# Optimization experiments

Measured on AMD Instinct MI355X. Metric: run time of the kernel, lower is better.

## Reference

```python
import jax, jax.numpy as jnp
import numpy as np

VOCAB, EMB, HID = 128000, 128, 1024
B, S = 4, 4096

def setup_inputs() -> dict:
    key = jax.random.key(0)
    k1, k2, k3 = jax.random.split(key, 3)
    x = jax.random.randint(k1, (B, S), 0, VOCAB, dtype=jnp.int64)
    embed_vocab = jax.random.normal(k2, (VOCAB, EMB), dtype=jnp.float32)
    embed_hidden = jax.random.normal(k3, (EMB, HID), dtype=jnp.float32)
    return {"x": x, "embed_vocab": embed_vocab, "embed_hidden": embed_hidden}

def reference(x, embed_vocab, embed_hidden):
    # Faithful to the torch module: build the full factorized table [V,H]
    # then gather rows by token id (F.embedding with defaults: no padding_idx,
    # no max_norm).
    table = embed_vocab @ embed_hidden          # [V, H]
    return jnp.take(table, x, axis=0)           # [B, S, H]
```

## Files before the change

kernel.cpp:

```cpp
#include <hip/hip_runtime.h>


using f32x4 = __attribute__((ext_vector_type(4))) float;
using i32x4 = __attribute__((ext_vector_type(4))) int;
typedef unsigned int u32;

constexpr int EMB = 128;
constexpr int HID = 1024;

__device__ inline void cvt8(const float f[8], i32x4& hi, i32x4& lo) {
    u32 h[8], l[8];
#pragma unroll
    for (int e = 0; e < 8; ++e) {
        u32 fb = __float_as_uint(f[e]);
        u32 hb = fb & 0xFFFF0000u;
        float r = f[e] - __uint_as_float(hb);
        u32 lb = __float_as_uint(r) & 0xFFFF0000u;
        h[e] = hb; l[e] = lb;
    }
#pragma unroll
    for (int p = 0; p < 4; ++p) {
        hi[p] = (int)((h[2*p] >> 16) | h[2*p+1]);
        lo[p] = (int)((l[2*p] >> 16) | l[2*p+1]);
    }
}

__device__ inline f32x4 mfma_bf16(i32x4 a, i32x4 b, f32x4 c) {
    f32x4 d;
    asm volatile("v_mfma_f32_16x16x32_bf16 %0, %1, %2, %3"
                 : "=&v"(d) : "v"(a), "v"(b), "v"(c));
    return d;
}

__device__ inline void gload16(const u32* src, u32* ldsdst) {
    __builtin_amdgcn_global_load_lds(
        (const __attribute__((address_space(1))) u32*)src,
        (__attribute__((address_space(3))) u32*)ldsdst, 16, 0, 0);
}

__global__ void prep_eh(const float* __restrict__ eh, u32* __restrict__ wsBh,
                        u32* __restrict__ wsBl) {
    const int t  = blockIdx.x * 256 + threadIdx.x;
    const int n  = t >> 4, k8 = t & 15;
    float f[8];
#pragma unroll
    for (int j = 0; j < 8; ++j) f[j] = eh[(k8*8 + j)*HID + n];
    i32x4 hi, lo; cvt8(f, hi, lo);
    const int s = k8 >> 2, gs = (k8 & 3) ^ ((n >> 1) & 3);
    const int off = (s*HID + n)*16 + gs*4;
    *(i32x4*)(wsBh + off) = hi;
    *(i32x4*)(wsBl + off) = lo;
}

__global__ void prep_ev(const int* __restrict__ x, const float* __restrict__ ev,
                        u32* __restrict__ wsAh, u32* __restrict__ wsAl, int M) {
    const int t = blockIdx.x * 256 + threadIdx.x;
    const int m = t >> 4, k8 = t & 15;
    const long id = x[m];
    const float* src = ev + id * EMB + k8*8;
    float f[8];
    *(float4*)(f)     = *(const float4*)(src);
    *(float4*)(f + 4) = *(const float4*)(src + 4);
    i32x4 hi, lo; cvt8(f, hi, lo);
    const int s = k8 >> 2, gs = (k8 & 3) ^ ((m >> 1) & 3);
    const long off = ((long)s*M + m)*16 + gs*4;
    *(i32x4*)(wsAh + off) = hi;
    *(i32x4*)(wsAl + off) = lo;
}

__global__ __launch_bounds__(256, 2)
void femb_main(const u32* __restrict__ wsAh, const u32* __restrict__ wsAl,
               const u32* __restrict__ wsBh, const u32* __restrict__ wsBl,
               float* __restrict__ out, int mtiles, int M)
{
    __shared__ __align__(16) u32 lds[2][4][2048];

    const int tid  = threadIdx.x;
    const int lane = tid & 63, wid = tid >> 6;
    const int bid  = blockIdx.x;
    const int mt   = bid % mtiles;
    const int nt   = bid / mtiles;
    const long m0  = (long)mt * 128, n0 = (long)nt * 128;
    const int wm   = wid >> 1, wn = wid & 1;
    const int rl   = lane & 15, g = lane >> 4;

    const int row_ = wid*32 + (lane >> 2);
    const int gr_  = lane & 3;

    f32x4 acc[4][4];
#pragma unroll
    for (int i = 0; i < 4; ++i)
#pragma unroll
        for (int j = 0; j < 4; ++j) acc[i][j] = (f32x4){0.f, 0.f, 0.f, 0.f};

    auto stage = [&](int s, int buf) {
#pragma unroll
        for (int j = 0; j < 2; ++j) {
            const int  r  = row_ + j*16;
            const int  lo = wid*512 + j*256;
            const long ao = ((long)s*M   + m0 + r)*16 + gr_*4;
            const long bo = ((long)s*HID + n0 + r)*16 + gr_*4;
            gload16(wsAh + ao, &lds[buf][0][lo]);
            gload16(wsAl + ao, &lds[buf][1][lo]);
            gload16(wsBh + bo, &lds[buf][2][lo]);
            gload16(wsBl + bo, &lds[buf][3][lo]);
        }
    };

    auto compute = [&](int buf) {
        i32x4 bh[4], bl[4];
#pragma unroll
        for (int nf = 0; nf < 4; ++nf) {
            const int nr  = wn*64 + nf*16 + rl;
            const int off = nr*16 + ((g ^ ((nr >> 1) & 3)) << 2);
            bh[nf] = *(const i32x4*)&lds[buf][2][off];
            bl[nf] = *(const i32x4*)&lds[buf][3][off];
        }
#pragma unroll
        for (int mf = 0; mf < 4; ++mf) {
            const int mr  = wm*64 + mf*16 + rl;
            const int off = mr*16 + ((g ^ ((mr >> 1) & 3)) << 2);
            const i32x4 ah = *(const i32x4*)&lds[buf][0][off];
            const i32x4 al = *(const i32x4*)&lds[buf][1][off];
#pragma unroll
            for (int nf = 0; nf < 4; ++nf) {
                acc[mf][nf] = mfma_bf16(ah, bh[nf], acc[mf][nf]);
                acc[mf][nf] = mfma_bf16(ah, bl[nf], acc[mf][nf]);
                acc[mf][nf] = mfma_bf16(al, bh[nf], acc[mf][nf]);
            }
        }
    };

    stage(0, 0);
    for (int s = 0; s < 4; ++s) {
        __builtin_amdgcn_s_waitcnt(0);
        __syncthreads();
        if (s < 3) stage(s + 1, (s + 1) & 1);
        compute(s & 1);
    }

#pragma unroll
    for (int mf = 0; mf < 4; ++mf)
#pragma unroll
        for (int j = 0; j < 4; ++j) {
            const long row = m0 + wm*64 + mf*16 + g*4 + j;
            float* dst = out + row * HID + n0 + wn*64 + rl;
#pragma unroll
            for (int nf = 0; nf < 4; ++nf) dst[nf * 16] = acc[mf][nf][j];
        }
}

extern "C" void kernel_launch(void* const* d_in, const int* in_sizes, int n_in,
                              void* d_out, int out_size, void* d_ws, size_t ws_size,
                              hipStream_t stream) {
    const int*   x   = (const int*)d_in[0];
    const float* ev  = (const float*)d_in[1];
    const float* eh  = (const float*)d_in[2];
    float*       out = (float*)d_out;

    const int M      = in_sizes[0];
    const int mtiles = M / 128;

    u32* wsBh = (u32*)d_ws;
    u32* wsBl = wsBh + (size_t)HID*64;
    u32* wsAh = wsBl + (size_t)HID*64;
    u32* wsAl = wsAh + (size_t)M*64;
    if (ws_size < (size_t)(2*HID*64 + 2*(size_t)M*64) * 4) return;

    prep_eh<<<HID*16/256, 256, 0, stream>>>(eh, wsBh, wsBl);
    prep_ev<<<M*16/256, 256, 0, stream>>>(x, ev, wsAh, wsAl, M);
    femb_main<<<mtiles * (HID/128), 256, 0, stream>>>(wsAh, wsAl, wsBh, wsBl,
                                                      out, mtiles, M);
}
```

Measured before the change: 123.6 us.

## Merge prep kernels and enlarge GEMM tiles to 256x256 with 1024-thread blocks

The two preprocessing kernels become one launch that splits blocks between the embedding-gather path and the hidden-weight conversion path, removing one kernel launch. The main kernel moves from 128x128 tiles with 4 waves to 256x256 tiles with 16 waves per block, doubling LDS use and reusing each staged operand across more MFMAs. Block indices are remapped so groups of 8 M-tiles share N-tiles, for better L2 locality. The trade-off is fewer, larger blocks (256 total), which may underfill the CUs and limit occupancy, since only one block fits per CU.

```diff
diff --git a/kernel.cpp b/kernel.cpp
--- a/kernel.cpp
+++ b/kernel.cpp
@@ -38,54 +38,54 @@
         (__attribute__((address_space(3))) u32*)ldsdst, 16, 0, 0);
 }
 
-__global__ void prep_eh(const float* __restrict__ eh, u32* __restrict__ wsBh,
-                        u32* __restrict__ wsBl) {
-    const int t  = blockIdx.x * 256 + threadIdx.x;
-    const int n  = t >> 4, k8 = t & 15;
-    float f[8];
+__global__ void prep_all(const int* __restrict__ x, const float* __restrict__ ev,
+                         const float* __restrict__ eh,
+                         u32* __restrict__ wsAh, u32* __restrict__ wsAl,
+                         u32* __restrict__ wsBh, u32* __restrict__ wsBl, int M) {
+    const int bid = blockIdx.x;
+    const int evblocks = M >> 4;
+    if (bid < evblocks) {
+        const int t = bid * 256 + threadIdx.x;
+        const int m = t >> 4, k8 = t & 15;
+        const long id = x[m];
+        const float* src = ev + id * EMB + k8 * 8;
+        float f[8];
+        *(float4*)(f)     = *(const float4*)(src);
+        *(float4*)(f + 4) = *(const float4*)(src + 4);
+        i32x4 hi, lo; cvt8(f, hi, lo);
+        const int s = k8 >> 2, gs = (k8 & 3) ^ ((m >> 1) & 3);
+        const long off = ((long)s * M + m) * 16 + gs * 4;
+        *(i32x4*)(wsAh + off) = hi;
+        *(i32x4*)(wsAl + off) = lo;
+    } else {
+        const int t = (bid - evblocks) * 256 + threadIdx.x;
+        const int n = t >> 4, k8 = t & 15;
+        float f[8];
 #pragma unroll
-    for (int j = 0; j < 8; ++j) f[j] = eh[(k8*8 + j)*HID + n];
-    i32x4 hi, lo; cvt8(f, hi, lo);
-    const int s = k8 >> 2, gs = (k8 & 3) ^ ((n >> 1) & 3);
-    const int off = (s*HID + n)*16 + gs*4;
-    *(i32x4*)(wsBh + off) = hi;
-    *(i32x4*)(wsBl + off) = lo;
+        for (int j = 0; j < 8; ++j) f[j] = eh[(k8 * 8 + j) * HID + n];
+        i32x4 hi, lo; cvt8(f, hi, lo);
+        const int s = k8 >> 2, gs = (k8 & 3) ^ ((n >> 1) & 3);
+        const int off = (s * HID + n) * 16 + gs * 4;
+        *(i32x4*)(wsBh + off) = hi;
+        *(i32x4*)(wsBl + off) = lo;
+    }
 }
 
-__global__ void prep_ev(const int* __restrict__ x, const float* __restrict__ ev,
-                        u32* __restrict__ wsAh, u32* __restrict__ wsAl, int M) {
-    const int t = blockIdx.x * 256 + threadIdx.x;
-    const int m = t >> 4, k8 = t & 15;
-    const long id = x[m];
-    const float* src = ev + id * EMB + k8*8;
-    float f[8];
-    *(float4*)(f)     = *(const float4*)(src);
-    *(float4*)(f + 4) = *(const float4*)(src + 4);
-    i32x4 hi, lo; cvt8(f, hi, lo);
-    const int s = k8 >> 2, gs = (k8 & 3) ^ ((m >> 1) & 3);
-    const long off = ((long)s*M + m)*16 + gs*4;
-    *(i32x4*)(wsAh + off) = hi;
-    *(i32x4*)(wsAl + off) = lo;
-}
-
-__global__ __launch_bounds__(256, 2)
+__global__ __launch_bounds__(1024, 1)
 void femb_main(const u32* __restrict__ wsAh, const u32* __restrict__ wsAl,
                const u32* __restrict__ wsBh, const u32* __restrict__ wsBl,
-               float* __restrict__ out, int mtiles, int M)
+               float* __restrict__ out, int M)
 {
-    __shared__ __align__(16) u32 lds[2][4][2048];
+    __shared__ __align__(16) u32 lds[2][4][4096];
 
     const int tid  = threadIdx.x;
     const int lane = tid & 63, wid = tid >> 6;
-    const int bid  = blockIdx.x;
-    const int mt   = bid % mtiles;
-    const int nt   = bid / mtiles;
-    const long m0  = (long)mt * 128, n0 = (long)nt * 128;
-    const int wm   = wid >> 1, wn = wid & 1;
-    const int rl   = lane & 15, g = lane >> 4;
-
-    const int row_ = wid*32 + (lane >> 2);
-    const int gr_  = lane & 3;
+    const int bid = blockIdx.x;
+    const int mh  = bid >> 5, r5 = bid & 31;
+    const int nt  = r5 >> 3,  mt = mh * 8 + (r5 & 7);
+    const long m0 = (long)mt * 256, n0 = (long)nt * 256;
+    const int wm  = wid >> 2, wn = wid & 3;
+    const int rl  = lane & 15, g = lane >> 4;
 
     f32x4 acc[4][4];
 #pragma unroll
@@ -94,32 +94,27 @@
         for (int j = 0; j < 4; ++j) acc[i][j] = (f32x4){0.f, 0.f, 0.f, 0.f};
 
     auto stage = [&](int s, int buf) {
-#pragma unroll
-        for (int j = 0; j < 2; ++j) {
-            const int  r  = row_ + j*16;
-            const int  lo = wid*512 + j*256;
-            const long ao = ((long)s*M   + m0 + r)*16 + gr_*4;
-            const long bo = ((long)s*HID + n0 + r)*16 + gr_*4;
-            gload16(wsAh + ao, &lds[buf][0][lo]);
-            gload16(wsAl + ao, &lds[buf][1][lo]);
-            gload16(wsBh + bo, &lds[buf][2][lo]);
-            gload16(wsBl + bo, &lds[buf][3][lo]);
-        }
+        const long ao = ((long)s * M   + m0) * 16 + tid * 4;
+        const long bo = ((long)s * HID + n0) * 16 + tid * 4;
+        gload16(wsAh + ao, &lds[buf][0][tid * 4]);
+        gload16(wsAl + ao, &lds[buf][1][tid * 4]);
+        gload16(wsBh + bo, &lds[buf][2][tid * 4]);
+        gload16(wsBl + bo, &lds[buf][3][tid * 4]);
     };
 
     auto compute = [&](int buf) {
         i32x4 bh[4], bl[4];
 #pragma unroll
         for (int nf = 0; nf < 4; ++nf) {
-            const int nr  = wn*64 + nf*16 + rl;
-            const int off = nr*16 + ((g ^ ((nr >> 1) & 3)) << 2);
+            const int nr  = wn * 64 + nf * 16 + rl;
+            const int off = nr * 16 + ((g ^ ((nr >> 1) & 3)) << 2);
             bh[nf] = *(const i32x4*)&lds[buf][2][off];
             bl[nf] = *(const i32x4*)&lds[buf][3][off];
         }
 #pragma unroll
         for (int mf = 0; mf < 4; ++mf) {
-            const int mr  = wm*64 + mf*16 + rl;
-            const int off = mr*16 + ((g ^ ((mr >> 1) & 3)) << 2);
+            const int mr  = wm * 64 + mf * 16 + rl;
+            const int off = mr * 16 + ((g ^ ((mr >> 1) & 3)) << 2);
             const i32x4 ah = *(const i32x4*)&lds[buf][0][off];
             const i32x4 al = *(const i32x4*)&lds[buf][1][off];
 #pragma unroll
@@ -143,8 +138,8 @@
     for (int mf = 0; mf < 4; ++mf)
 #pragma unroll
         for (int j = 0; j < 4; ++j) {
-            const long row = m0 + wm*64 + mf*16 + g*4 + j;
-            float* dst = out + row * HID + n0 + wn*64 + rl;
+            const long row = m0 + wm * 64 + mf * 16 + g * 4 + j;
+            float* dst = out + row * HID + n0 + wn * 64 + rl;
 #pragma unroll
             for (int nf = 0; nf < 4; ++nf) dst[nf * 16] = acc[mf][nf][j];
         }
@@ -158,17 +153,16 @@
     const float* eh  = (const float*)d_in[2];
     float*       out = (float*)d_out;
 
-    const int M      = in_sizes[0];
-    const int mtiles = M / 128;
+    const int M = in_sizes[0];
 
     u32* wsBh = (u32*)d_ws;
-    u32* wsBl = wsBh + (size_t)HID*64;
-    u32* wsAh = wsBl + (size_t)HID*64;
-    u32* wsAl = wsAh + (size_t)M*64;
-    if (ws_size < (size_t)(2*HID*64 + 2*(size_t)M*64) * 4) return;
+    u32* wsBl = wsBh + (size_t)HID * 64;
+    u32* wsAh = wsBl + (size_t)HID * 64;
+    u32* wsAl = wsAh + (size_t)M * 64;
+    if (ws_size < (size_t)(2 * HID * 64 + 2 * (size_t)M * 64) * 4) return;
 
-    prep_eh<<<HID*16/256, 256, 0, stream>>>(eh, wsBh, wsBl);
-    prep_ev<<<M*16/256, 256, 0, stream>>>(x, ev, wsAh, wsAl, M);
-    femb_main<<<mtiles * (HID/128), 256, 0, stream>>>(wsAh, wsAl, wsBh, wsBl,
-                                                      out, mtiles, M);
+    prep_all<<<(M >> 4) + (HID * 16 / 256), 256, 0, stream>>>(
+        x, ev, eh, wsAh, wsAl, wsBh, wsBl, M);
+    femb_main<<<(M / 256) * (HID / 256), 1024, 0, stream>>>(
+        wsAh, wsAl, wsBh, wsBl, out, M);
 }
```

Result: slower. 126.7 us (+2.5%).

## Fuse gather and bf16 split conversion into main GEMM kernel, drop prep passes

Applied to the files above, without the earlier changes.

Removes the two prep kernels that wrote split-bf16 hi/lo copies of the gathered embedding rows and the hidden matrix to workspace. The main kernel now gathers fp32 rows by token id, loads columns of embed_hidden, converts them to hi/lo in registers, and writes them to LDS. Global loads for the next stage are issued before the MFMA compute and stored to LDS after it, so the pipeline moves from async global-to-LDS copies to register staging. This saves two launches and the workspace round trip. The cost is redundant conversion across the 8 N-tiles, strided uncoalesced column reads of embed_hidden, and higher register pressure.

```diff
diff --git a/kernel.cpp b/kernel.cpp
--- a/kernel.cpp
+++ b/kernel.cpp
@@ -32,46 +32,9 @@
     return d;
 }
 
-__device__ inline void gload16(const u32* src, u32* ldsdst) {
-    __builtin_amdgcn_global_load_lds(
-        (const __attribute__((address_space(1))) u32*)src,
-        (__attribute__((address_space(3))) u32*)ldsdst, 16, 0, 0);
-}
-
-__global__ void prep_eh(const float* __restrict__ eh, u32* __restrict__ wsBh,
-                        u32* __restrict__ wsBl) {
-    const int t  = blockIdx.x * 256 + threadIdx.x;
-    const int n  = t >> 4, k8 = t & 15;
-    float f[8];
-#pragma unroll
-    for (int j = 0; j < 8; ++j) f[j] = eh[(k8*8 + j)*HID + n];
-    i32x4 hi, lo; cvt8(f, hi, lo);
-    const int s = k8 >> 2, gs = (k8 & 3) ^ ((n >> 1) & 3);
-    const int off = (s*HID + n)*16 + gs*4;
-    *(i32x4*)(wsBh + off) = hi;
-    *(i32x4*)(wsBl + off) = lo;
-}
-
-__global__ void prep_ev(const int* __restrict__ x, const float* __restrict__ ev,
-                        u32* __restrict__ wsAh, u32* __restrict__ wsAl, int M) {
-    const int t = blockIdx.x * 256 + threadIdx.x;
-    const int m = t >> 4, k8 = t & 15;
-    const long id = x[m];
-    const float* src = ev + id * EMB + k8*8;
-    float f[8];
-    *(float4*)(f)     = *(const float4*)(src);
-    *(float4*)(f + 4) = *(const float4*)(src + 4);
-    i32x4 hi, lo; cvt8(f, hi, lo);
-    const int s = k8 >> 2, gs = (k8 & 3) ^ ((m >> 1) & 3);
-    const long off = ((long)s*M + m)*16 + gs*4;
-    *(i32x4*)(wsAh + off) = hi;
-    *(i32x4*)(wsAl + off) = lo;
-}
-
 __global__ __launch_bounds__(256, 2)
-void femb_main(const u32* __restrict__ wsAh, const u32* __restrict__ wsAl,
-               const u32* __restrict__ wsBh, const u32* __restrict__ wsBl,
-               float* __restrict__ out, int mtiles, int M)
+void femb(const int* __restrict__ x, const float* __restrict__ ev,
+          const float* __restrict__ eh, float* __restrict__ out, int mtiles)
 {
     __shared__ __align__(16) u32 lds[2][4][2048];
 
@@ -84,8 +47,49 @@
     const int wm   = wid >> 1, wn = wid & 1;
     const int rl   = lane & 15, g = lane >> 4;
 
-    const int row_ = wid*32 + (lane >> 2);
-    const int gr_  = lane & 3;
+    const int r0 = tid >> 2, aoct = tid & 3;
+    const float* abase0 = ev + (long)x[m0 + r0]      * EMB + aoct * 8;
+    const float* abase1 = ev + (long)x[m0 + 64 + r0] * EMB + aoct * 8;
+    const int bn = tid & 127, boct0 = tid >> 7;
+    const float* bcol = eh + n0 + bn;
+
+    float af[2][8], bf[2][8];
+
+    auto loads = [&](int s) {
+        const int k0 = s * 32;
+#pragma unroll
+        for (int h = 0; h < 2; ++h) {
+            const float* src = (h ? abase1 : abase0) + k0;
+            *(float4*)(&af[h][0]) = *(const float4*)(src);
+            *(float4*)(&af[h][4]) = *(const float4*)(src + 4);
+        }
+#pragma unroll
+        for (int h = 0; h < 2; ++h) {
+            const int ko = k0 + (boct0 + 2 * h) * 8;
+#pragma unroll
+            for (int j = 0; j < 8; ++j)
+                bf[h][j] = bcol[(long)(ko + j) * HID];
+        }
+    };
+
+    auto cvtwrite = [&](int buf) {
+#pragma unroll
+        for (int h = 0; h < 2; ++h) {
+            i32x4 hi, lo; cvt8(af[h], hi, lo);
+            const int r  = r0 + h * 64;
+            const int gs = aoct ^ ((r >> 1) & 3);
+            *(i32x4*)&lds[buf][0][r * 16 + gs * 4] = hi;
+            *(i32x4*)&lds[buf][1][r * 16 + gs * 4] = lo;
+        }
+#pragma unroll
+        for (int h = 0; h < 2; ++h) {
+            i32x4 hi, lo; cvt8(bf[h], hi, lo);
+            const int o  = boct0 + 2 * h;
+            const int gs = o ^ ((bn >> 1) & 3);
+            *(i32x4*)&lds[buf][2][bn * 16 + gs * 4] = hi;
+            *(i32x4*)&lds[buf][3][bn * 16 + gs * 4] = lo;
+        }
+    };
 
     f32x4 acc[4][4];
 #pragma unroll
@@ -93,33 +97,19 @@
 #pragma unroll
         for (int j = 0; j < 4; ++j) acc[i][j] = (f32x4){0.f, 0.f, 0.f, 0.f};
 
-    auto stage = [&](int s, int buf) {
-#pragma unroll
-        for (int j = 0; j < 2; ++j) {
-            const int  r  = row_ + j*16;
-            const int  lo = wid*512 + j*256;
-            const long ao = ((long)s*M   + m0 + r)*16 + gr_*4;
-            const long bo = ((long)s*HID + n0 + r)*16 + gr_*4;
-            gload16(wsAh + ao, &lds[buf][0][lo]);
-            gload16(wsAl + ao, &lds[buf][1][lo]);
-            gload16(wsBh + bo, &lds[buf][2][lo]);
-            gload16(wsBl + bo, &lds[buf][3][lo]);
-        }
-    };
-
     auto compute = [&](int buf) {
         i32x4 bh[4], bl[4];
 #pragma unroll
         for (int nf = 0; nf < 4; ++nf) {
-            const int nr  = wn*64 + nf*16 + rl;
-            const int off = nr*16 + ((g ^ ((nr >> 1) & 3)) << 2);
+            const int nr  = wn * 64 + nf * 16 + rl;
+            const int off = nr * 16 + ((g ^ ((nr >> 1) & 3)) << 2);
             bh[nf] = *(const i32x4*)&lds[buf][2][off];
             bl[nf] = *(const i32x4*)&lds[buf][3][off];
         }
 #pragma unroll
         for (int mf = 0; mf < 4; ++mf) {
-            const int mr  = wm*64 + mf*16 + rl;
-            const int off = mr*16 + ((g ^ ((mr >> 1) & 3)) << 2);
+            const int mr  = wm * 64 + mf * 16 + rl;
+            const int off = mr * 16 + ((g ^ ((mr >> 1) & 3)) << 2);
             const i32x4 ah = *(const i32x4*)&lds[buf][0][off];
             const i32x4 al = *(const i32x4*)&lds[buf][1][off];
 #pragma unroll
@@ -131,20 +121,26 @@
         }
     };
 
-    stage(0, 0);
+    loads(0);
+    cvtwrite(0);
+    __builtin_amdgcn_s_waitcnt(0);
+    __syncthreads();
+
+#pragma unroll
     for (int s = 0; s < 4; ++s) {
+        if (s < 3) loads(s + 1);
+        compute(s & 1);
+        if (s < 3) cvtwrite((s + 1) & 1);
         __builtin_amdgcn_s_waitcnt(0);
         __syncthreads();
-        if (s < 3) stage(s + 1, (s + 1) & 1);
-        compute(s & 1);
     }
 
 #pragma unroll
     for (int mf = 0; mf < 4; ++mf)
 #pragma unroll
         for (int j = 0; j < 4; ++j) {
-            const long row = m0 + wm*64 + mf*16 + g*4 + j;
-            float* dst = out + row * HID + n0 + wn*64 + rl;
+            const long row = m0 + wm * 64 + mf * 16 + g * 4 + j;
+            float* dst = out + row * HID + n0 + wn * 64 + rl;
 #pragma unroll
             for (int nf = 0; nf < 4; ++nf) dst[nf * 16] = acc[mf][nf][j];
         }
@@ -161,14 +157,5 @@
     const int M      = in_sizes[0];
     const int mtiles = M / 128;
 
-    u32* wsBh = (u32*)d_ws;
-    u32* wsBl = wsBh + (size_t)HID*64;
-    u32* wsAh = wsBl + (size_t)HID*64;
-    u32* wsAl = wsAh + (size_t)M*64;
-    if (ws_size < (size_t)(2*HID*64 + 2*(size_t)M*64) * 4) return;
-
-    prep_eh<<<HID*16/256, 256, 0, stream>>>(eh, wsBh, wsBl);
-    prep_ev<<<M*16/256, 256, 0, stream>>>(x, ev, wsAh, wsAl, M);
-    femb_main<<<mtiles * (HID/128), 256, 0, stream>>>(wsAh, wsAl, wsBh, wsBl,
-                                                      out, mtiles, M);
+    femb<<<mtiles * (HID / 128), 256, 0, stream>>>(x, ev, eh, out, mtiles);
 }
```

Result: no change. 121.4 us (-1.8%).
